# Kernel tuning notes

Hardware: AMD Instinct MI355X
Metric: run time of the kernel (lower is better)

## Reference

```python
import jax, jax.numpy as jnp
import numpy as np

N_NODES = 100000
N_EDGES = 640000
D = 128
L = 3
NUM_GRAPHS = 128


def setup_inputs() -> dict:
    key = jax.random.key(0)
    ks = jax.random.split(key, 8)
    scale = 1.0 / np.sqrt(D)
    x = jax.random.normal(ks[0], (N_NODES, D), dtype=jnp.float32)
    edge_index = jax.random.randint(ks[1], (2, N_EDGES), 0, N_NODES, dtype=jnp.int64)
    batch = jnp.sort(jax.random.randint(ks[2], (N_NODES,), 0, NUM_GRAPHS, dtype=jnp.int64))
    W1 = jax.random.normal(ks[3], (L, D, D), dtype=jnp.float32) * scale
    b1 = jnp.zeros((L, D), dtype=jnp.float32)
    W2 = jax.random.normal(ks[4], (L, D, D), dtype=jnp.float32) * scale
    b2 = jnp.zeros((L, D), dtype=jnp.float32)
    return {"x": x, "edge_index": edge_index, "batch": batch,
            "W1": W1, "b1": b1, "W2": W2, "b2": b2}


def reference(x, edge_index, batch, W1, b1, W2, b2):
    # GIN forward: per layer z = ReLU(MLP((1+eps)*z + sum_{j in N(i)} z_j)), eps=0
    n = x.shape[0]
    src, dst = edge_index[0], edge_index[1]  # messages flow src -> dst
    z = x
    for l in range(W1.shape[0]):
        agg = jax.ops.segment_sum(z[src], dst, num_segments=n)  # scatter-add aggregation
        h = agg + z                                             # (1+eps)*x_i + sum x_j, eps=0
        h = jnp.maximum(h @ W1[l] + b1[l], 0.0)                 # Linear + ReLU
        z = h @ W2[l] + b2[l]                                   # Linear
        z = jnp.maximum(z, 0.0)                                 # F.relu after conv
    # global mean pool over graph ids (dropout is identity in eval / p=0)
    ones = jnp.ones((n,), dtype=z.dtype)
    counts = jax.ops.segment_sum(ones, batch, num_segments=NUM_GRAPHS)
    sums = jax.ops.segment_sum(z, batch, num_segments=NUM_GRAPHS)
    g = sums / jnp.maximum(counts, 1.0)[:, None]
    return z, g
```

## Files before the change

### kernel.cpp

```cpp
#include <hip/hip_runtime.h>
#include <hip/hip_bf16.h>

#define D 128
#define NG 128

typedef __attribute__((ext_vector_type(8))) short bf16x8;
typedef __attribute__((ext_vector_type(4))) float f32x4;

__device__ inline unsigned short f2bf(float f) {
  union { float f; unsigned u; } c; c.f = f;
  unsigned u = c.u;
  return (unsigned short)((u + 0x7FFFu + ((u >> 16) & 1u)) >> 16);
}
__device__ inline float bf2f(unsigned short b) {
  union { unsigned u; float f; } c; c.u = ((unsigned)b) << 16;
  return c.f;
}

__global__ void prep_w(const float* __restrict__ W1, const float* __restrict__ W2,
                       unsigned short* __restrict__ Wt1, unsigned short* __restrict__ Wt2,
                       int* __restrict__ deg, int N, float* __restrict__ g) {
  int t = blockIdx.x * 256 + threadIdx.x;
  if (t < N) deg[t] = 0;
  if (t < NG * D) g[t] = 0.f;
  if (t >= 3 * 128 * 128) return;
  int l = t >> 14, k = (t >> 7) & 127, n = t & 127;
  int o = (l << 14) + (n << 7) + k;
  Wt1[o] = f2bf(W1[t]);
  Wt2[o] = f2bf(W2[t]);
}


__global__ void hist_deg(const int* __restrict__ dst, int* __restrict__ deg, int E) {
  int e = blockIdx.x * 256 + threadIdx.x;
  if (e < E) atomicAdd(deg + dst[e], 1);
}

__global__ __launch_bounds__(256) void scan1(const int* __restrict__ deg,
    int* __restrict__ rowptr, int* __restrict__ bsum, int n) {
  __shared__ int sh[256];
  int tid = threadIdx.x;
  int idx = blockIdx.x * 1024 + tid * 4;
  int v[4], tsum = 0;
#pragma unroll
  for (int j = 0; j < 4; ++j) { v[j] = (idx + j < n) ? deg[idx + j] : 0; tsum += v[j]; }
  sh[tid] = tsum;
  __syncthreads();
  for (int off = 1; off < 256; off <<= 1) {
    int x = (tid >= off) ? sh[tid - off] : 0;
    __syncthreads();
    sh[tid] += x;
    __syncthreads();
  }
  if (tid == 255) bsum[blockIdx.x] = sh[255];
  int run = sh[tid] - tsum;
#pragma unroll
  for (int j = 0; j < 4; ++j) { if (idx + j < n) rowptr[idx + j] = run; run += v[j]; }
}

__global__ __launch_bounds__(128) void scan2(int* __restrict__ bsum, int nb) {
  __shared__ int sh[128];
  int tid = threadIdx.x;
  int v = (tid < nb) ? bsum[tid] : 0;
  sh[tid] = v;
  __syncthreads();
  for (int off = 1; off < 128; off <<= 1) {
    int x = (tid >= off) ? sh[tid - off] : 0;
    __syncthreads();
    sh[tid] += x;
    __syncthreads();
  }
  if (tid < nb) bsum[tid] = sh[tid] - v;
}

__global__ void scan3(int* __restrict__ rowptr, int* __restrict__ pos,
                      const int* __restrict__ bsum, int n, int E) {
  int t = blockIdx.x * 256 + threadIdx.x;
  if (t < n) {
    int v = rowptr[t] + bsum[t >> 10];
    rowptr[t] = v;
    pos[t] = v;
  }
  if (t == 0) rowptr[n] = E;
}

__global__ void edge_scatter(const int* __restrict__ src, const int* __restrict__ dst,
                             int* __restrict__ pos, int* __restrict__ csr_src, int E) {
  int e = blockIdx.x * 256 + threadIdx.x;
  if (e >= E) return;
  int idx = atomicAdd(pos + dst[e], 1);
  csr_src[idx] = src[e];
}


template<bool IN_BF16>
__global__ __launch_bounds__(256) void gather_agg(const void* __restrict__ zin,
    const int* __restrict__ rowptr, const int* __restrict__ csr_src,
    unsigned short* __restrict__ agg, int N) {
  int t = blockIdx.x * 256 + threadIdx.x;
  int node = t >> 3;
  if (node >= N) return;
  int c = (t & 7) * 16;
  const float* zf = (const float*)zin;
  const unsigned short* zb = (const unsigned short*)zin;

  float acc[16];

  if constexpr (IN_BF16) {
    const unsigned short* p = zb + (size_t)node * D + c;
    bf16x8 v0 = *(const bf16x8*)(p);
    bf16x8 v1 = *(const bf16x8*)(p + 8);
#pragma unroll
    for (int j = 0; j < 8; ++j) {
      acc[j]     = bf2f((unsigned short)v0[j]);
      acc[j + 8] = bf2f((unsigned short)v1[j]);
    }
  } else {
    const float* p = zf + (size_t)node * D + c;
    float4 v0 = *(const float4*)(p);
    float4 v1 = *(const float4*)(p + 4);
    float4 v2 = *(const float4*)(p + 8);
    float4 v3 = *(const float4*)(p + 12);
    acc[0]  = v0.x; acc[1]  = v0.y; acc[2]  = v0.z; acc[3]  = v0.w;
    acc[4]  = v1.x; acc[5]  = v1.y; acc[6]  = v1.z; acc[7]  = v1.w;
    acc[8]  = v2.x; acc[9]  = v2.y; acc[10] = v2.z; acc[11] = v2.w;
    acc[12] = v3.x; acc[13] = v3.y; acc[14] = v3.z; acc[15] = v3.w;
  }

  int e  = rowptr[node];
  int e1 = rowptr[node + 1];

  if constexpr (IN_BF16) {
    for (; e + 4 <= e1; e += 4) {
      int s0 = csr_src[e + 0];
      int s1 = csr_src[e + 1];
      int s2 = csr_src[e + 2];
      int s3 = csr_src[e + 3];
      const unsigned short* p0 = zb + (size_t)s0 * D + c;
      const unsigned short* p1 = zb + (size_t)s1 * D + c;
      const unsigned short* p2 = zb + (size_t)s2 * D + c;
      const unsigned short* p3 = zb + (size_t)s3 * D + c;
      bf16x8 a0 = *(const bf16x8*)(p0), a1 = *(const bf16x8*)(p0 + 8);
      bf16x8 b0 = *(const bf16x8*)(p1), b1 = *(const bf16x8*)(p1 + 8);
      bf16x8 c0 = *(const bf16x8*)(p2), c1 = *(const bf16x8*)(p2 + 8);
      bf16x8 d0 = *(const bf16x8*)(p3), d1 = *(const bf16x8*)(p3 + 8);
#pragma unroll
      for (int j = 0; j < 8; ++j) {
        acc[j]     += (bf2f((unsigned short)a0[j]) + bf2f((unsigned short)b0[j]))
                    + (bf2f((unsigned short)c0[j]) + bf2f((unsigned short)d0[j]));
        acc[j + 8] += (bf2f((unsigned short)a1[j]) + bf2f((unsigned short)b1[j]))
                    + (bf2f((unsigned short)c1[j]) + bf2f((unsigned short)d1[j]));
      }
    }
    if (e + 2 <= e1) {
      int s0 = csr_src[e + 0];
      int s1 = csr_src[e + 1];
      const unsigned short* p0 = zb + (size_t)s0 * D + c;
      const unsigned short* p1 = zb + (size_t)s1 * D + c;
      bf16x8 a0 = *(const bf16x8*)(p0), a1 = *(const bf16x8*)(p0 + 8);
      bf16x8 b0 = *(const bf16x8*)(p1), b1 = *(const bf16x8*)(p1 + 8);
#pragma unroll
      for (int j = 0; j < 8; ++j) {
        acc[j]     += bf2f((unsigned short)a0[j]) + bf2f((unsigned short)b0[j]);
        acc[j + 8] += bf2f((unsigned short)a1[j]) + bf2f((unsigned short)b1[j]);
      }
      e += 2;
    }
    if (e < e1) {
      int s0 = csr_src[e];
      const unsigned short* p0 = zb + (size_t)s0 * D + c;
      bf16x8 a0 = *(const bf16x8*)(p0), a1 = *(const bf16x8*)(p0 + 8);
#pragma unroll
      for (int j = 0; j < 8; ++j) {
        acc[j]     += bf2f((unsigned short)a0[j]);
        acc[j + 8] += bf2f((unsigned short)a1[j]);
      }
    }
  } else {
    for (; e + 2 <= e1; e += 2) {
      int s0 = csr_src[e + 0];
      int s1 = csr_src[e + 1];
      const float* p0 = zf + (size_t)s0 * D + c;
      const float* p1 = zf + (size_t)s1 * D + c;
      float4 u0 = *(const float4*)(p0);
      float4 u1 = *(const float4*)(p0 + 4);
      float4 u2 = *(const float4*)(p0 + 8);
      float4 u3 = *(const float4*)(p0 + 12);
      float4 w0 = *(const float4*)(p1);
      float4 w1 = *(const float4*)(p1 + 4);
      float4 w2 = *(const float4*)(p1 + 8);
      float4 w3 = *(const float4*)(p1 + 12);
      acc[0]  += u0.x + w0.x; acc[1]  += u0.y + w0.y;
      acc[2]  += u0.z + w0.z; acc[3]  += u0.w + w0.w;
      acc[4]  += u1.x + w1.x; acc[5]  += u1.y + w1.y;
      acc[6]  += u1.z + w1.z; acc[7]  += u1.w + w1.w;
      acc[8]  += u2.x + w2.x; acc[9]  += u2.y + w2.y;
      acc[10] += u2.z + w2.z; acc[11] += u2.w + w2.w;
      acc[12] += u3.x + w3.x; acc[13] += u3.y + w3.y;
      acc[14] += u3.z + w3.z; acc[15] += u3.w + w3.w;
    }
    if (e < e1) {
      int s0 = csr_src[e];
      const float* p0 = zf + (size_t)s0 * D + c;
      float4 u0 = *(const float4*)(p0);
      float4 u1 = *(const float4*)(p0 + 4);
      float4 u2 = *(const float4*)(p0 + 8);
      float4 u3 = *(const float4*)(p0 + 12);
      acc[0]  += u0.x; acc[1]  += u0.y; acc[2]  += u0.z; acc[3]  += u0.w;
      acc[4]  += u1.x; acc[5]  += u1.y; acc[6]  += u1.z; acc[7]  += u1.w;
      acc[8]  += u2.x; acc[9]  += u2.y; acc[10] += u2.z; acc[11] += u2.w;
      acc[12] += u3.x; acc[13] += u3.y; acc[14] += u3.z; acc[15] += u3.w;
    }
  }

  bf16x8 o0, o1;
#pragma unroll
  for (int j = 0; j < 8; ++j) {
    o0[j] = (short)f2bf(acc[j]);
    o1[j] = (short)f2bf(acc[j + 8]);
  }
  unsigned short* q = agg + (size_t)node * D + c;
  *(bf16x8*)(q)     = o0;
  *(bf16x8*)(q + 8) = o1;
}


template<bool LAST>
__global__ __launch_bounds__(256) void gemm_fused(const unsigned short* __restrict__ A,
    const unsigned short* __restrict__ Wt1, const float* __restrict__ b1v,
    const unsigned short* __restrict__ Wt2, const float* __restrict__ b2v,
    unsigned short* __restrict__ Zb, float* __restrict__ Zf, int M) {
  __shared__ unsigned short hs[4][32][136];
  int lane = threadIdx.x & 63;
  int wid  = threadIdx.x >> 6;
  int row_base = blockIdx.x * 128 + wid * 32;
  int c16 = lane & 15;
  int kq  = lane >> 4;
  int koff = kq * 8;

  bf16x8 a[2][4];
#pragma unroll
  for (int fr = 0; fr < 2; ++fr) {
    int row = row_base + fr * 16 + c16;
    row = row < M ? row : M - 1;
#pragma unroll
    for (int kk = 0; kk < 4; ++kk)
      a[fr][kk] = *(const bf16x8*)(A + (size_t)row * D + kk * 32 + koff);
  }

  bf16x8 bf[8][4];
  float  bb[8];
#pragma unroll
  for (int fc = 0; fc < 8; ++fc) {
    bb[fc] = b1v[fc * 16 + c16];
#pragma unroll
    for (int kk = 0; kk < 4; ++kk)
      bf[fc][kk] = *(const bf16x8*)(Wt1 + (size_t)(fc * 16 + c16) * D + kk * 32 + koff);
  }

#pragma unroll
  for (int fc = 0; fc < 8; ++fc) {
    f32x4 acc0 = {0.f, 0.f, 0.f, 0.f};
    f32x4 acc1 = {0.f, 0.f, 0.f, 0.f};
    int col = fc * 16 + c16;
#pragma unroll
    for (int kk = 0; kk < 4; ++kk) {
      acc0 = __builtin_amdgcn_mfma_f32_16x16x32_bf16(a[0][kk], bf[fc][kk], acc0, 0, 0, 0);
      acc1 = __builtin_amdgcn_mfma_f32_16x16x32_bf16(a[1][kk], bf[fc][kk], acc1, 0, 0, 0);
    }
#pragma unroll
    for (int r = 0; r < 4; ++r) {
      int rl = kq * 4 + r;
      hs[wid][rl][col]      = f2bf(fmaxf(acc0[r] + bb[fc], 0.f));
      hs[wid][rl + 16][col] = f2bf(fmaxf(acc1[r] + bb[fc], 0.f));
    }
  }
  __syncthreads();

  bf16x8 a2[2][4];
#pragma unroll
  for (int fr = 0; fr < 2; ++fr)
#pragma unroll
    for (int kk = 0; kk < 4; ++kk)
      a2[fr][kk] = *(const bf16x8*)&hs[wid][fr * 16 + c16][kk * 32 + koff];

#pragma unroll
  for (int fc = 0; fc < 8; ++fc) {
    bb[fc] = b2v[fc * 16 + c16];
#pragma unroll
    for (int kk = 0; kk < 4; ++kk)
      bf[fc][kk] = *(const bf16x8*)(Wt2 + (size_t)(fc * 16 + c16) * D + kk * 32 + koff);
  }

#pragma unroll
  for (int fc = 0; fc < 8; ++fc) {
    f32x4 acc0 = {0.f, 0.f, 0.f, 0.f};
    f32x4 acc1 = {0.f, 0.f, 0.f, 0.f};
    int col = fc * 16 + c16;
#pragma unroll
    for (int kk = 0; kk < 4; ++kk) {
      acc0 = __builtin_amdgcn_mfma_f32_16x16x32_bf16(a2[0][kk], bf[fc][kk], acc0, 0, 0, 0);
      acc1 = __builtin_amdgcn_mfma_f32_16x16x32_bf16(a2[1][kk], bf[fc][kk], acc1, 0, 0, 0);
    }
#pragma unroll
    for (int r = 0; r < 4; ++r) {
      int row0 = row_base + kq * 4 + r;
      float v0 = fmaxf(acc0[r] + bb[fc], 0.f);
      if (row0 < M) {
        if constexpr (LAST) Zf[(size_t)row0 * D + col] = v0;
        else                Zb[(size_t)row0 * D + col] = f2bf(v0);
      }
      int row1 = row0 + 16;
      float v1 = fmaxf(acc1[r] + bb[fc], 0.f);
      if (row1 < M) {
        if constexpr (LAST) Zf[(size_t)row1 * D + col] = v1;
        else                Zb[(size_t)row1 * D + col] = f2bf(v1);
      }
    }
  }
}


__global__ __launch_bounds__(128) void pool_bounds(const int* __restrict__ batch,
                                                   int* __restrict__ start, int N) {
  int g = threadIdx.x;
  int lo = 0, hi = N;
  while (lo < hi) {
    int mid = (lo + hi) >> 1;
    if (batch[mid] < g) lo = mid + 1; else hi = mid;
  }
  start[g] = lo;
  if (g == 0) start[NG] = N;
}

#define PCHUNKS 8
__global__ __launch_bounds__(128) void pool_mean(const float* __restrict__ z,
    const int* __restrict__ start, float* __restrict__ g) {
  int gid   = blockIdx.x >> 3;
  int chunk = blockIdx.x & (PCHUNKS - 1);
  int col = threadIdx.x;
  int s = start[gid], epos = start[gid + 1];
  int len = epos - s;
  if (len <= 0) return;
  int per = (len + PCHUNKS - 1) / PCHUNKS;
  int r0 = s + chunk * per;
  int r1 = min(r0 + per, epos);
  if (r0 >= r1) return;
  float a0 = 0.f, a1 = 0.f, a2 = 0.f, a3 = 0.f;
  int i = r0;
  for (; i + 4 <= r1; i += 4) {
    a0 += z[(size_t)(i + 0) * D + col];
    a1 += z[(size_t)(i + 1) * D + col];
    a2 += z[(size_t)(i + 2) * D + col];
    a3 += z[(size_t)(i + 3) * D + col];
  }
  for (; i < r1; ++i) a0 += z[(size_t)i * D + col];
  atomicAdd(g + (size_t)gid * D + col, (a0 + a1) + (a2 + a3));
}

__global__ void pool_div(float* __restrict__ g, const int* __restrict__ start) {
  int t = blockIdx.x * 256 + threadIdx.x;
  if (t >= NG * D) return;
  int gid = t >> 7;
  int cnt = start[gid + 1] - start[gid];
  g[t] = g[t] / fmaxf((float)cnt, 1.f);
}

extern "C" void kernel_launch(void* const* d_in, const int* in_sizes, int n_in,
                              void* d_out, int out_size, void* d_ws, size_t ws_size,
                              hipStream_t stream) {
  const float* x     = (const float*)d_in[0];
  const int*   ei    = (const int*)d_in[1];
  const int*   batch = (const int*)d_in[2];
  const float* W1    = (const float*)d_in[3];
  const float* b1    = (const float*)d_in[4];
  const float* W2    = (const float*)d_in[5];
  const float* b2    = (const float*)d_in[6];

  const int N = in_sizes[0] / D;
  const int E = in_sizes[1] / 2;
  const int* src = ei;
  const int* dst = ei + E;

  float* zout = (float*)d_out;
  float* g    = zout + (size_t)N * D;

  char* w = (char*)d_ws;
  unsigned short* agg     = (unsigned short*)w;    w += (size_t)N * D * 2;
  unsigned short* zb      = (unsigned short*)w;    w += (size_t)N * D * 2;
  unsigned short* Wt1     = (unsigned short*)w;    w += 3 * 16384 * 2;
  unsigned short* Wt2     = (unsigned short*)w;    w += 3 * 16384 * 2;
  int*            start   = (int*)w;               w += (NG + 4) * 4;
  int*            deg     = (int*)w;               w += (size_t)N * 4;
  int*            rowptr  = (int*)w;               w += (size_t)(N + 4) * 4;
  int*            pos     = (int*)w;               w += (size_t)N * 4;
  int*            bsum    = (int*)w;               w += 128 * 4;
  int*            csr_src = (int*)w;               w += (size_t)E * 4;

  const int nb = (N + 1023) / 1024;

  int prep_threads = (3 * 128 * 128 > N) ? 3 * 128 * 128 : N;
  prep_w<<<(prep_threads + 255) / 256, 256, 0, stream>>>(W1, W2, Wt1, Wt2, deg, N, g);

  pool_bounds<<<1, 128, 0, stream>>>(batch, start, N);

  hist_deg<<<(E + 255) / 256, 256, 0, stream>>>(dst, deg, E);
  scan1<<<nb, 256, 0, stream>>>(deg, rowptr, bsum, N);
  scan2<<<1, 128, 0, stream>>>(bsum, nb);
  scan3<<<(N + 255) / 256, 256, 0, stream>>>(rowptr, pos, bsum, N, E);
  edge_scatter<<<(E + 255) / 256, 256, 0, stream>>>(src, dst, pos, csr_src, E);

  const int gather_blocks = (int)(((size_t)N * 8 + 255) / 256);
  const int gemm_blocks   = (N + 127) / 128;

  gather_agg<false><<<gather_blocks, 256, 0, stream>>>(x, rowptr, csr_src, agg, N);
  gemm_fused<false><<<gemm_blocks, 256, 0, stream>>>(agg, Wt1, b1, Wt2, b2, zb, zout, N);
  gather_agg<true><<<gather_blocks, 256, 0, stream>>>(zb, rowptr, csr_src, agg, N);
  gemm_fused<false><<<gemm_blocks, 256, 0, stream>>>(agg, Wt1 + 16384, b1 + 128,
                                                     Wt2 + 16384, b2 + 128, zb, zout, N);
  gather_agg<true><<<gather_blocks, 256, 0, stream>>>(zb, rowptr, csr_src, agg, N);
  gemm_fused<true><<<gemm_blocks, 256, 0, stream>>>(agg, Wt1 + 32768, b1 + 256,
                                                    Wt2 + 32768, b2 + 256, zb, zout, N);

  pool_mean<<<NG * PCHUNKS, 128, 0, stream>>>(zout, start, g);
  pool_div<<<(NG * D + 255) / 256, 256, 0, stream>>>(g, start);
}
```

Measured before the change: 336.0 us.

## Store node features in column panels and gather per panel with edge-parallel lanes

Node features are now stored as eight column panels of 16 bf16 values each, so that each gather block only touches a 3.2 MB panel that fits in cache. The GEMM epilogue writes into this panel layout, and a new prep kernel converts x to bf16 panels ahead of the first layer. The gather now spreads a node's edges across 8 lanes, reduces them with shuffles, and uses nontemporal loads and stores. The trade-offs are an extra conversion pass over x, strided scattered epilogue stores, and a shuffle reduction.

```diff
diff --git a/kernel.cpp b/kernel.cpp
--- a/kernel.cpp
+++ b/kernel.cpp
@@ -30,6 +30,29 @@
   Wt2[o] = f2bf(W2[t]);
 }
 
+__global__ void prep_xp(const float* __restrict__ x, unsigned short* __restrict__ xp, int N) {
+  int t = blockIdx.x * 256 + threadIdx.x;
+  if (t >= N * 8) return;
+  int n = t >> 3, p = t & 7;
+  const float* src = x + (size_t)n * D + p * 16;
+  float4 v0 = *(const float4*)(src);
+  float4 v1 = *(const float4*)(src + 4);
+  float4 v2 = *(const float4*)(src + 8);
+  float4 v3 = *(const float4*)(src + 12);
+  bf16x8 o0, o1;
+  o0[0] = (short)f2bf(v0.x); o0[1] = (short)f2bf(v0.y);
+  o0[2] = (short)f2bf(v0.z); o0[3] = (short)f2bf(v0.w);
+  o0[4] = (short)f2bf(v1.x); o0[5] = (short)f2bf(v1.y);
+  o0[6] = (short)f2bf(v1.z); o0[7] = (short)f2bf(v1.w);
+  o1[0] = (short)f2bf(v2.x); o1[1] = (short)f2bf(v2.y);
+  o1[2] = (short)f2bf(v2.z); o1[3] = (short)f2bf(v2.w);
+  o1[4] = (short)f2bf(v3.x); o1[5] = (short)f2bf(v3.y);
+  o1[6] = (short)f2bf(v3.z); o1[7] = (short)f2bf(v3.w);
+  unsigned short* dstp = xp + (size_t)p * N * 16 + (size_t)n * 16;
+  *(bf16x8*)(dstp)     = o0;
+  *(bf16x8*)(dstp + 8) = o1;
+}
+
 
 __global__ void hist_deg(const int* __restrict__ dst, int* __restrict__ deg, int E) {
   int e = blockIdx.x * 256 + threadIdx.x;
@@ -93,135 +116,49 @@
 }
 
 
-template<bool IN_BF16>
-__global__ __launch_bounds__(256) void gather_agg(const void* __restrict__ zin,
+__global__ __launch_bounds__(256) void gather_panel(const unsigned short* __restrict__ zp,
     const int* __restrict__ rowptr, const int* __restrict__ csr_src,
     unsigned short* __restrict__ agg, int N) {
-  int t = blockIdx.x * 256 + threadIdx.x;
-  int node = t >> 3;
-  if (node >= N) return;
-  int c = (t & 7) * 16;
-  const float* zf = (const float*)zin;
-  const unsigned short* zb = (const unsigned short*)zin;
+  int tid = threadIdx.x;
+  int p = blockIdx.x & 7;
+  int grp = tid >> 3;
+  int li  = tid & 7;
+  int n = (blockIdx.x >> 3) * 32 + grp;
+  if (n >= N) return;
+  const unsigned short* panel = zp + (size_t)p * N * 16;
+
+  int e0 = rowptr[n], e1 = rowptr[n + 1];
+  int cnt = e1 - e0 + 1;
 
   float acc[16];
-
-  if constexpr (IN_BF16) {
-    const unsigned short* p = zb + (size_t)node * D + c;
-    bf16x8 v0 = *(const bf16x8*)(p);
-    bf16x8 v1 = *(const bf16x8*)(p + 8);
+#pragma unroll
+  for (int j = 0; j < 16; ++j) acc[j] = 0.f;
+
+  for (int i = li; i < cnt; i += 8) {
+    int s = (i == 0) ? n : __builtin_nontemporal_load(csr_src + e0 + i - 1);
+    const unsigned short* q = panel + (size_t)s * 16;
+    bf16x8 v0 = *(const bf16x8*)(q);
+    bf16x8 v1 = *(const bf16x8*)(q + 8);
 #pragma unroll
     for (int j = 0; j < 8; ++j) {
-      acc[j]     = bf2f((unsigned short)v0[j]);
-      acc[j + 8] = bf2f((unsigned short)v1[j]);
-    }
-  } else {
-    const float* p = zf + (size_t)node * D + c;
-    float4 v0 = *(const float4*)(p);
-    float4 v1 = *(const float4*)(p + 4);
-    float4 v2 = *(const float4*)(p + 8);
-    float4 v3 = *(const float4*)(p + 12);
-    acc[0]  = v0.x; acc[1]  = v0.y; acc[2]  = v0.z; acc[3]  = v0.w;
-    acc[4]  = v1.x; acc[5]  = v1.y; acc[6]  = v1.z; acc[7]  = v1.w;
-    acc[8]  = v2.x; acc[9]  = v2.y; acc[10] = v2.z; acc[11] = v2.w;
-    acc[12] = v3.x; acc[13] = v3.y; acc[14] = v3.z; acc[15] = v3.w;
-  }
-
-  int e  = rowptr[node];
-  int e1 = rowptr[node + 1];
-
-  if constexpr (IN_BF16) {
-    for (; e + 4 <= e1; e += 4) {
-      int s0 = csr_src[e + 0];
-      int s1 = csr_src[e + 1];
-      int s2 = csr_src[e + 2];
-      int s3 = csr_src[e + 3];
-      const unsigned short* p0 = zb + (size_t)s0 * D + c;
-      const unsigned short* p1 = zb + (size_t)s1 * D + c;
-      const unsigned short* p2 = zb + (size_t)s2 * D + c;
-      const unsigned short* p3 = zb + (size_t)s3 * D + c;
-      bf16x8 a0 = *(const bf16x8*)(p0), a1 = *(const bf16x8*)(p0 + 8);
-      bf16x8 b0 = *(const bf16x8*)(p1), b1 = *(const bf16x8*)(p1 + 8);
-      bf16x8 c0 = *(const bf16x8*)(p2), c1 = *(const bf16x8*)(p2 + 8);
-      bf16x8 d0 = *(const bf16x8*)(p3), d1 = *(const bf16x8*)(p3 + 8);
-#pragma unroll
-      for (int j = 0; j < 8; ++j) {
-        acc[j]     += (bf2f((unsigned short)a0[j]) + bf2f((unsigned short)b0[j]))
-                    + (bf2f((unsigned short)c0[j]) + bf2f((unsigned short)d0[j]));
-        acc[j + 8] += (bf2f((unsigned short)a1[j]) + bf2f((unsigned short)b1[j]))
-                    + (bf2f((unsigned short)c1[j]) + bf2f((unsigned short)d1[j]));
-      }
-    }
-    if (e + 2 <= e1) {
-      int s0 = csr_src[e + 0];
-      int s1 = csr_src[e + 1];
-      const unsigned short* p0 = zb + (size_t)s0 * D + c;
-      const unsigned short* p1 = zb + (size_t)s1 * D + c;
-      bf16x8 a0 = *(const bf16x8*)(p0), a1 = *(const bf16x8*)(p0 + 8);
-      bf16x8 b0 = *(const bf16x8*)(p1), b1 = *(const bf16x8*)(p1 + 8);
-#pragma unroll
-      for (int j = 0; j < 8; ++j) {
-        acc[j]     += bf2f((unsigned short)a0[j]) + bf2f((unsigned short)b0[j]);
-        acc[j + 8] += bf2f((unsigned short)a1[j]) + bf2f((unsigned short)b1[j]);
-      }
-      e += 2;
-    }
-    if (e < e1) {
-      int s0 = csr_src[e];
-      const unsigned short* p0 = zb + (size_t)s0 * D + c;
-      bf16x8 a0 = *(const bf16x8*)(p0), a1 = *(const bf16x8*)(p0 + 8);
-#pragma unroll
-      for (int j = 0; j < 8; ++j) {
-        acc[j]     += bf2f((unsigned short)a0[j]);
-        acc[j + 8] += bf2f((unsigned short)a1[j]);
-      }
-    }
-  } else {
-    for (; e + 2 <= e1; e += 2) {
-      int s0 = csr_src[e + 0];
-      int s1 = csr_src[e + 1];
-      const float* p0 = zf + (size_t)s0 * D + c;
-      const float* p1 = zf + (size_t)s1 * D + c;
-      float4 u0 = *(const float4*)(p0);
-      float4 u1 = *(const float4*)(p0 + 4);
-      float4 u2 = *(const float4*)(p0 + 8);
-      float4 u3 = *(const float4*)(p0 + 12);
-      float4 w0 = *(const float4*)(p1);
-      float4 w1 = *(const float4*)(p1 + 4);
-      float4 w2 = *(const float4*)(p1 + 8);
-      float4 w3 = *(const float4*)(p1 + 12);
-      acc[0]  += u0.x + w0.x; acc[1]  += u0.y + w0.y;
-      acc[2]  += u0.z + w0.z; acc[3]  += u0.w + w0.w;
-      acc[4]  += u1.x + w1.x; acc[5]  += u1.y + w1.y;
-      acc[6]  += u1.z + w1.z; acc[7]  += u1.w + w1.w;
-      acc[8]  += u2.x + w2.x; acc[9]  += u2.y + w2.y;
-      acc[10] += u2.z + w2.z; acc[11] += u2.w + w2.w;
-      acc[12] += u3.x + w3.x; acc[13] += u3.y + w3.y;
-      acc[14] += u3.z + w3.z; acc[15] += u3.w + w3.w;
-    }
-    if (e < e1) {
-      int s0 = csr_src[e];
-      const float* p0 = zf + (size_t)s0 * D + c;
-      float4 u0 = *(const float4*)(p0);
-      float4 u1 = *(const float4*)(p0 + 4);
-      float4 u2 = *(const float4*)(p0 + 8);
-      float4 u3 = *(const float4*)(p0 + 12);
-      acc[0]  += u0.x; acc[1]  += u0.y; acc[2]  += u0.z; acc[3]  += u0.w;
-      acc[4]  += u1.x; acc[5]  += u1.y; acc[6]  += u1.z; acc[7]  += u1.w;
-      acc[8]  += u2.x; acc[9]  += u2.y; acc[10] += u2.z; acc[11] += u2.w;
-      acc[12] += u3.x; acc[13] += u3.y; acc[14] += u3.z; acc[15] += u3.w;
-    }
-  }
-
-  bf16x8 o0, o1;
-#pragma unroll
-  for (int j = 0; j < 8; ++j) {
-    o0[j] = (short)f2bf(acc[j]);
-    o1[j] = (short)f2bf(acc[j + 8]);
-  }
-  unsigned short* q = agg + (size_t)node * D + c;
-  *(bf16x8*)(q)     = o0;
-  *(bf16x8*)(q + 8) = o1;
+      acc[j]     += bf2f((unsigned short)v0[j]);
+      acc[j + 8] += bf2f((unsigned short)v1[j]);
+    }
+  }
+
+#pragma unroll
+  for (int off = 1; off < 8; off <<= 1) {
+#pragma unroll
+    for (int j = 0; j < 16; ++j)
+      acc[j] += __shfl_xor(acc[j], off, 64);
+  }
+
+  if (li < 2) {
+    bf16x8 o;
+#pragma unroll
+    for (int j = 0; j < 8; ++j) o[j] = (short)f2bf(acc[li * 8 + j]);
+    __builtin_nontemporal_store(o, (bf16x8*)(agg + (size_t)n * D + p * 16 + li * 8));
+  }
 }
 
 
@@ -302,19 +239,21 @@
       acc0 = __builtin_amdgcn_mfma_f32_16x16x32_bf16(a2[0][kk], bf[fc][kk], acc0, 0, 0, 0);
       acc1 = __builtin_amdgcn_mfma_f32_16x16x32_bf16(a2[1][kk], bf[fc][kk], acc1, 0, 0, 0);
     }
+    int pp  = col >> 4;
+    int off = col & 15;
 #pragma unroll
     for (int r = 0; r < 4; ++r) {
       int row0 = row_base + kq * 4 + r;
       float v0 = fmaxf(acc0[r] + bb[fc], 0.f);
       if (row0 < M) {
         if constexpr (LAST) Zf[(size_t)row0 * D + col] = v0;
-        else                Zb[(size_t)row0 * D + col] = f2bf(v0);
+        else                Zb[(size_t)pp * M * 16 + (size_t)row0 * 16 + off] = f2bf(v0);
       }
       int row1 = row0 + 16;
       float v1 = fmaxf(acc1[r] + bb[fc], 0.f);
       if (row1 < M) {
         if constexpr (LAST) Zf[(size_t)row1 * D + col] = v1;
-        else                Zb[(size_t)row1 * D + col] = f2bf(v1);
+        else                Zb[(size_t)pp * M * 16 + (size_t)row1 * 16 + off] = f2bf(v1);
       }
     }
   }
@@ -387,7 +326,8 @@
 
   char* w = (char*)d_ws;
   unsigned short* agg     = (unsigned short*)w;    w += (size_t)N * D * 2;
-  unsigned short* zb      = (unsigned short*)w;    w += (size_t)N * D * 2;
+  unsigned short* zp      = (unsigned short*)w;    w += (size_t)N * D * 2;
+  unsigned short* xp      = (unsigned short*)w;    w += (size_t)N * D * 2;
   unsigned short* Wt1     = (unsigned short*)w;    w += 3 * 16384 * 2;
   unsigned short* Wt2     = (unsigned short*)w;    w += 3 * 16384 * 2;
   int*            start   = (int*)w;               w += (NG + 4) * 4;
@@ -401,6 +341,7 @@
 
   int prep_threads = (3 * 128 * 128 > N) ? 3 * 128 * 128 : N;
   prep_w<<<(prep_threads + 255) / 256, 256, 0, stream>>>(W1, W2, Wt1, Wt2, deg, N, g);
+  prep_xp<<<(N * 8 + 255) / 256, 256, 0, stream>>>(x, xp, N);
 
   pool_bounds<<<1, 128, 0, stream>>>(batch, start, N);
 
@@ -410,17 +351,17 @@
   scan3<<<(N + 255) / 256, 256, 0, stream>>>(rowptr, pos, bsum, N, E);
   edge_scatter<<<(E + 255) / 256, 256, 0, stream>>>(src, dst, pos, csr_src, E);
 
-  const int gather_blocks = (int)(((size_t)N * 8 + 255) / 256);
+  const int gather_blocks = 8 * ((N + 31) / 32);
   const int gemm_blocks   = (N + 127) / 128;
 
-  gather_agg<false><<<gather_blocks, 256, 0, stream>>>(x, rowptr, csr_src, agg, N);
-  gemm_fused<false><<<gemm_blocks, 256, 0, stream>>>(agg, Wt1, b1, Wt2, b2, zb, zout, N);
-  gather_agg<true><<<gather_blocks, 256, 0, stream>>>(zb, rowptr, csr_src, agg, N);
+  gather_panel<<<gather_blocks, 256, 0, stream>>>(xp, rowptr, csr_src, agg, N);
+  gemm_fused<false><<<gemm_blocks, 256, 0, stream>>>(agg, Wt1, b1, Wt2, b2, zp, zout, N);
+  gather_panel<<<gather_blocks, 256, 0, stream>>>(zp, rowptr, csr_src, agg, N);
   gemm_fused<false><<<gemm_blocks, 256, 0, stream>>>(agg, Wt1 + 16384, b1 + 128,
-                                                     Wt2 + 16384, b2 + 128, zb, zout, N);
-  gather_agg<true><<<gather_blocks, 256, 0, stream>>>(zb, rowptr, csr_src, agg, N);
+                                                     Wt2 + 16384, b2 + 128, zp, zout, N);
+  gather_panel<<<gather_blocks, 256, 0, stream>>>(zp, rowptr, csr_src, agg, N);
   gemm_fused<true><<<gemm_blocks, 256, 0, stream>>>(agg, Wt1 + 32768, b1 + 256,
-                                                    Wt2 + 32768, b2 + 256, zb, zout, N);
+                                                    Wt2 + 32768, b2 + 256, zp, zout, N);
 
   pool_mean<<<NG * PCHUNKS, 128, 0, stream>>>(zout, start, g);
   pool_div<<<(NG * D + 255) / 256, 256, 0, stream>>>(g, start);
```

Result: slower. 489.2 us (+45.6%).

## Restructure fused MLP GEMM: two tiles per block, W2 in LDS, coalesced stores

Applied to the files above, without the earlier changes.

The fused two-layer MLP kernel now processes two 128-row tiles per block and works on 16-row halves. W1 fragments are held in registers and W2 is staged once in shared memory, so weight loads are amortised across more rows. The next tile's A operand is prefetched while the current half computes, and bf16 outputs go through LDS so they can be written as 16-byte coalesced stores. The cost is half as many blocks, a larger LDS footprint, and a launch_bounds occupancy hint of 2 blocks per CU that may add register pressure.

```diff
diff --git a/kernel.cpp b/kernel.cpp
--- a/kernel.cpp
+++ b/kernel.cpp
@@ -226,97 +226,111 @@
 
 
 template<bool LAST>
-__global__ __launch_bounds__(256) void gemm_fused(const unsigned short* __restrict__ A,
+__global__ __launch_bounds__(256, 2) void gemm_fused(const unsigned short* __restrict__ A,
     const unsigned short* __restrict__ Wt1, const float* __restrict__ b1v,
     const unsigned short* __restrict__ Wt2, const float* __restrict__ b2v,
-    unsigned short* __restrict__ Zb, float* __restrict__ Zf, int M) {
-  __shared__ unsigned short hs[4][32][136];
-  int lane = threadIdx.x & 63;
-  int wid  = threadIdx.x >> 6;
-  int row_base = blockIdx.x * 128 + wid * 32;
-  int c16 = lane & 15;
-  int kq  = lane >> 4;
+    unsigned short* __restrict__ Zb, float* __restrict__ Zf, int M, int nt) {
+  __shared__ unsigned short w2s[128][136];
+  __shared__ unsigned short hs[4][16][136];
+  int tid  = threadIdx.x;
+  int lane = tid & 63;
+  int wid  = tid >> 6;
+  int c16  = lane & 15;
+  int kq   = lane >> 4;
   int koff = kq * 8;
 
-  bf16x8 a[2][4];
-#pragma unroll
-  for (int fr = 0; fr < 2; ++fr) {
-    int row = row_base + fr * 16 + c16;
-    row = row < M ? row : M - 1;
+#pragma unroll
+  for (int i = 0; i < 8; ++i) {
+    int chunk = i * 256 + tid;
+    int row = chunk >> 4, k16 = chunk & 15;
+    *(bf16x8*)&w2s[row][k16 * 8] = *(const bf16x8*)(Wt2 + (size_t)row * D + k16 * 8);
+  }
+
+  bf16x8 bf1[8][4];
+  float  bb1[8], bb2[8];
+#pragma unroll
+  for (int fc = 0; fc < 8; ++fc) {
+    int col = fc * 16 + c16;
+    bb1[fc] = b1v[col];
+    bb2[fc] = b2v[col];
 #pragma unroll
     for (int kk = 0; kk < 4; ++kk)
-      a[fr][kk] = *(const bf16x8*)(A + (size_t)row * D + kk * 32 + koff);
-  }
-
-  bf16x8 bf[8][4];
-  float  bb[8];
-#pragma unroll
-  for (int fc = 0; fc < 8; ++fc) {
-    bb[fc] = b1v[fc * 16 + c16];
+      bf1[fc][kk] = *(const bf16x8*)(Wt1 + (size_t)col * D + kk * 32 + koff);
+  }
+
+  int tile0 = blockIdx.x * 2;
+  int tile1 = tile0 + 1;
+
+  auto LOADA = [&](bf16x8 (&dst)[2][4], int tile) {
+#pragma unroll
+    for (int h = 0; h < 2; ++h) {
+      int row = tile * 128 + wid * 32 + h * 16 + c16;
+      row = row < M ? row : M - 1;
+#pragma unroll
+      for (int kk = 0; kk < 4; ++kk)
+        dst[h][kk] = *(const bf16x8*)(A + (size_t)row * D + kk * 32 + koff);
+    }
+  };
+
+  bf16x8 aA[2][4], aB[2][4];
+  LOADA(aA, tile0);
+  __syncthreads();
+
+  auto DO_HALF = [&](const bf16x8 (&a)[4], int rb) {
+#pragma unroll
+    for (int fc = 0; fc < 8; ++fc) {
+      f32x4 acc = {0.f, 0.f, 0.f, 0.f};
+#pragma unroll
+      for (int kk = 0; kk < 4; ++kk)
+        acc = __builtin_amdgcn_mfma_f32_16x16x32_bf16(a[kk], bf1[fc][kk], acc, 0, 0, 0);
+      int col = fc * 16 + c16;
+#pragma unroll
+      for (int r = 0; r < 4; ++r)
+        hs[wid][kq * 4 + r][col] = f2bf(fmaxf(acc[r] + bb1[fc], 0.f));
+    }
+    bf16x8 a2[4];
 #pragma unroll
     for (int kk = 0; kk < 4; ++kk)
-      bf[fc][kk] = *(const bf16x8*)(Wt1 + (size_t)(fc * 16 + c16) * D + kk * 32 + koff);
-  }
-
-#pragma unroll
-  for (int fc = 0; fc < 8; ++fc) {
-    f32x4 acc0 = {0.f, 0.f, 0.f, 0.f};
-    f32x4 acc1 = {0.f, 0.f, 0.f, 0.f};
-    int col = fc * 16 + c16;
-#pragma unroll
-    for (int kk = 0; kk < 4; ++kk) {
-      acc0 = __builtin_amdgcn_mfma_f32_16x16x32_bf16(a[0][kk], bf[fc][kk], acc0, 0, 0, 0);
-      acc1 = __builtin_amdgcn_mfma_f32_16x16x32_bf16(a[1][kk], bf[fc][kk], acc1, 0, 0, 0);
-    }
-#pragma unroll
-    for (int r = 0; r < 4; ++r) {
-      int rl = kq * 4 + r;
-      hs[wid][rl][col]      = f2bf(fmaxf(acc0[r] + bb[fc], 0.f));
-      hs[wid][rl + 16][col] = f2bf(fmaxf(acc1[r] + bb[fc], 0.f));
-    }
-  }
-  __syncthreads();
-
-  bf16x8 a2[2][4];
-#pragma unroll
-  for (int fr = 0; fr < 2; ++fr)
-#pragma unroll
-    for (int kk = 0; kk < 4; ++kk)
-      a2[fr][kk] = *(const bf16x8*)&hs[wid][fr * 16 + c16][kk * 32 + koff];
-
-#pragma unroll
-  for (int fc = 0; fc < 8; ++fc) {
-    bb[fc] = b2v[fc * 16 + c16];
-#pragma unroll
-    for (int kk = 0; kk < 4; ++kk)
-      bf[fc][kk] = *(const bf16x8*)(Wt2 + (size_t)(fc * 16 + c16) * D + kk * 32 + koff);
-  }
-
-#pragma unroll
-  for (int fc = 0; fc < 8; ++fc) {
-    f32x4 acc0 = {0.f, 0.f, 0.f, 0.f};
-    f32x4 acc1 = {0.f, 0.f, 0.f, 0.f};
-    int col = fc * 16 + c16;
-#pragma unroll
-    for (int kk = 0; kk < 4; ++kk) {
-      acc0 = __builtin_amdgcn_mfma_f32_16x16x32_bf16(a2[0][kk], bf[fc][kk], acc0, 0, 0, 0);
-      acc1 = __builtin_amdgcn_mfma_f32_16x16x32_bf16(a2[1][kk], bf[fc][kk], acc1, 0, 0, 0);
-    }
-#pragma unroll
-    for (int r = 0; r < 4; ++r) {
-      int row0 = row_base + kq * 4 + r;
-      float v0 = fmaxf(acc0[r] + bb[fc], 0.f);
-      if (row0 < M) {
-        if constexpr (LAST) Zf[(size_t)row0 * D + col] = v0;
-        else                Zb[(size_t)row0 * D + col] = f2bf(v0);
-      }
-      int row1 = row0 + 16;
-      float v1 = fmaxf(acc1[r] + bb[fc], 0.f);
-      if (row1 < M) {
-        if constexpr (LAST) Zf[(size_t)row1 * D + col] = v1;
-        else                Zb[(size_t)row1 * D + col] = f2bf(v1);
-      }
-    }
+      a2[kk] = *(const bf16x8*)&hs[wid][c16][kk * 32 + koff];
+#pragma unroll
+    for (int fc = 0; fc < 8; ++fc) {
+      f32x4 acc = {0.f, 0.f, 0.f, 0.f};
+      int col = fc * 16 + c16;
+#pragma unroll
+      for (int kk = 0; kk < 4; ++kk) {
+        bf16x8 b = *(const bf16x8*)&w2s[col][kk * 32 + koff];
+        acc = __builtin_amdgcn_mfma_f32_16x16x32_bf16(a2[kk], b, acc, 0, 0, 0);
+      }
+      if constexpr (LAST) {
+#pragma unroll
+        for (int r = 0; r < 4; ++r) {
+          int row = rb + kq * 4 + r;
+          if (row < M) Zf[(size_t)row * D + col] = fmaxf(acc[r] + bb2[fc], 0.f);
+        }
+      } else {
+#pragma unroll
+        for (int r = 0; r < 4; ++r)
+          hs[wid][kq * 4 + r][col] = f2bf(fmaxf(acc[r] + bb2[fc], 0.f));
+      }
+    }
+    if constexpr (!LAST) {
+#pragma unroll
+      for (int i = 0; i < 4; ++i) {
+        int rl = i * 4 + kq;
+        bf16x8 v = *(const bf16x8*)&hs[wid][rl][c16 * 8];
+        int row = rb + rl;
+        if (row < M)
+          *(bf16x8*)(Zb + (size_t)row * D + c16 * 8) = v;
+      }
+    }
+  };
+
+  DO_HALF(aA[0], tile0 * 128 + wid * 32);
+  if (tile1 < nt) LOADA(aB, tile1);
+  DO_HALF(aA[1], tile0 * 128 + wid * 32 + 16);
+  if (tile1 < nt) {
+    DO_HALF(aB[0], tile1 * 128 + wid * 32);
+    DO_HALF(aB[1], tile1 * 128 + wid * 32 + 16);
   }
 }
 
@@ -411,16 +425,17 @@
   edge_scatter<<<(E + 255) / 256, 256, 0, stream>>>(src, dst, pos, csr_src, E);
 
   const int gather_blocks = (int)(((size_t)N * 8 + 255) / 256);
-  const int gemm_blocks   = (N + 127) / 128;
+  const int nt            = (N + 127) / 128;
+  const int gemm_blocks   = (nt + 1) / 2;
 
   gather_agg<false><<<gather_blocks, 256, 0, stream>>>(x, rowptr, csr_src, agg, N);
-  gemm_fused<false><<<gemm_blocks, 256, 0, stream>>>(agg, Wt1, b1, Wt2, b2, zb, zout, N);
+  gemm_fused<false><<<gemm_blocks, 256, 0, stream>>>(agg, Wt1, b1, Wt2, b2, zb, zout, N, nt);
   gather_agg<true><<<gather_blocks, 256, 0, stream>>>(zb, rowptr, csr_src, agg, N);
   gemm_fused<false><<<gemm_blocks, 256, 0, stream>>>(agg, Wt1 + 16384, b1 + 128,
-                                                     Wt2 + 16384, b2 + 128, zb, zout, N);
+                                                     Wt2 + 16384, b2 + 128, zb, zout, N, nt);
   gather_agg<true><<<gather_blocks, 256, 0, stream>>>(zb, rowptr, csr_src, agg, N);
   gemm_fused<true><<<gemm_blocks, 256, 0, stream>>>(agg, Wt1 + 32768, b1 + 256,
-                                                    Wt2 + 32768, b2 + 256, zb, zout, N);
+                                                    Wt2 + 32768, b2 + 256, zb, zout, N, nt);
 
   pool_mean<<<NG * PCHUNKS, 128, 0, stream>>>(zout, start, g);
   pool_div<<<(NG * D + 255) / 256, 256, 0, stream>>>(g, start);
```

New measurement: 289.4 us. -13.9%, faster.
